# Optimization experiments

Measured on AMD Instinct MI355X. Metric: run time of the kernel, lower is better.

Reference implementation:

```python
import jax, jax.numpy as jnp
import numpy as np

N_VISITS, N_PROC, N_MED = 64, 32, 16
V_DIAG, V_PROC, V_MED = 2000, 1500, 4000
EMB, EMB_FF = 256, 128


def _normalize(adj):
    # row-normalize(adj + I), matching GCN.normalize
    adj = adj + np.eye(adj.shape[0], dtype=np.float32)
    rs = adj.sum(1)
    rinv = np.where(rs > 0, 1.0 / rs, 0.0).astype(np.float32)
    return (adj * rinv[:, None]).astype(np.float32)


def setup_inputs() -> dict:
    key = jax.random.key(0)
    ks = jax.random.split(key, 24)
    rng = np.random.default_rng(0)
    ehr = (rng.random((V_MED, V_MED)) < 0.01).astype(np.float32)
    ddi = (rng.random((V_MED, V_MED)) < 0.01).astype(np.float32)
    s = 0.02
    return {
        'proc_codes': jax.random.randint(ks[0], (N_VISITS, N_PROC), 0, V_DIAG + V_PROC + 2),
        'med_codes': jax.random.randint(ks[1], (N_VISITS, N_MED), 0, V_MED),
        'emb_table': jax.random.normal(ks[2], (V_DIAG + V_PROC + 2, EMB_FF)) * s,
        'conv_w': jax.random.normal(ks[3], (3,)) * 0.3,
        'conv_b': jnp.zeros((1,)),
        'wq': jax.random.normal(ks[4], (EMB_FF, EMB)) * s,
        'wk': jax.random.normal(ks[5], (EMB_FF, EMB)) * s,
        'wv': jax.random.normal(ks[6], (EMB_FF, EMB)) * s,
        'wr': jax.random.normal(ks[7], (EMB, EMB)) * s,
        'alpha': jax.random.normal(ks[8], (EMB,)),
        'beta': jax.random.normal(ks[9], (EMB,)),
        'ehr_adj_norm': jnp.asarray(_normalize(ehr)),
        'ddi_adj_norm': jnp.asarray(_normalize(ddi)),
        'ddi_adj_raw': jnp.asarray(ddi),
        'ehr_w1': jax.random.normal(ks[10], (V_MED, EMB)) * s,
        'ehr_b1': jnp.zeros((EMB,)),
        'ehr_w2': jax.random.normal(ks[11], (EMB, EMB)) * s,
        'ehr_b2': jnp.zeros((EMB,)),
        'ddi_w1': jax.random.normal(ks[12], (V_MED, EMB)) * s,
        'ddi_b1': jnp.zeros((EMB,)),
        'ddi_w2': jax.random.normal(ks[13], (EMB, EMB)) * s,
        'ddi_b2': jnp.zeros((EMB,)),
        'inter': jax.random.normal(ks[14], (1,)) * 0.1,
        'out_w1': jax.random.normal(ks[15], (3 * EMB, 2 * EMB)) * s,
        'out_b1': jnp.zeros((2 * EMB,)),
        'out_w2': jax.random.normal(ks[16], (2 * EMB, V_MED)) * s,
        'out_b2': jnp.zeros((V_MED,)),
    }


def _fastformer(x, wq, wk, wv, wr, alpha, beta):
    # x: (1, n, EMB_FF); additive linear attention (all-ones mask => no-op)
    q = x @ wq  # (1, n, EMB)
    k = x @ wk
    v = x @ wv
    scale = EMB ** -0.5
    aw = jax.nn.softmax(q * alpha * scale, axis=-1)
    gq = jnp.sum(q * aw, axis=1)              # global query (1, EMB)
    p = gq[:, None, :] * k                    # (1, n, EMB)
    bw = jax.nn.softmax(p * beta * scale, axis=-1)
    gk = jnp.sum(p * bw, axis=1)              # global key (1, EMB)
    return (gk[:, None, :] * v) @ wr + q


def _gcn(adj, w1, b1, w2, b2):
    # input x = I, so first layer support is just w1
    h = jax.nn.relu(adj @ w1 + b1)
    return adj @ (h @ w2) + b2


def reference(proc_codes, med_codes, emb_table, conv_w, conv_b, wq, wk, wv, wr, alpha, beta,
              ehr_adj_norm, ddi_adj_norm, ddi_adj_raw,
              ehr_w1, ehr_b1, ehr_w2, ehr_b2, ddi_w1, ddi_b1, ddi_w2, ddi_b2,
              inter, out_w1, out_b1, out_w2, out_b2):
    n = proc_codes.shape[0]
    # per-admission mean embedding  (n, EMB_FF)
    i2 = emb_table[proc_codes].mean(axis=1)
    # Conv1d(1,1,k=3,same) over the feature dim, then ReLU
    xp = jnp.pad(i2, ((0, 0), (1, 1)))
    i2 = jax.nn.relu(conv_w[0] * xp[:, :-2] + conv_w[1] * xp[:, 1:-1] + conv_w[2] * xp[:, 2:] + conv_b)
    feat = _fastformer(i2[None], wq, wk, wv, wr, alpha, beta)[0]  # (n, EMB)
    query = feat[-1:]
    drug_memory = _gcn(ehr_adj_norm, ehr_w1, ehr_b1, ehr_w2, ehr_b2) \
        - _gcn(ddi_adj_norm, ddi_w1, ddi_b1, ddi_w2, ddi_b2) * inter[0]
    key_w1 = jax.nn.softmax(query @ drug_memory.T, axis=-1)   # (1, V_MED)
    fact1 = key_w1 @ drug_memory                              # (1, EMB)
    # history (len(input) > 1): multi-hot med history values
    history_keys = feat[:-1]
    hv = jnp.zeros((n - 1, V_MED), dtype=feat.dtype)
    hv = hv.at[jnp.arange(n - 1)[:, None], med_codes[:-1]].set(1.0)
    visit_w = jax.nn.softmax(query @ history_keys.T, axis=-1)
    fact2 = (visit_w @ hv) @ drug_memory
    h = jnp.concatenate([query, fact1, fact2], axis=-1)       # (1, 3*EMB)
    result = jax.nn.relu(h @ out_w1 + out_b1) @ out_w2 + out_b2
    sp = jax.nn.sigmoid(result)[0]
    batch_neg = 0.0005 * jnp.einsum('i,ij,j->', sp, ddi_adj_raw, sp)
    return result, batch_neg
```

## Files before the change

### kernel.cpp

```cpp
#include <hip/hip_runtime.h>
#include <hip/hip_bf16.h>

#define NV 64
#define NP 32
#define NM 16
#define VMED 4000
#define EMB 256
#define EMBFF 128
#define CAP 128


__device__ __forceinline__ float block_sum_256(float v, float* red) {
    int t = threadIdx.x;
    red[t] = v; __syncthreads();
    for (int s = 128; s > 0; s >>= 1) { if (t < s) red[t] += red[t + s]; __syncthreads(); }
    float r = red[0]; __syncthreads();
    return r;
}
__device__ __forceinline__ float block_max_256(float v, float* red) {
    int t = threadIdx.x;
    red[t] = v; __syncthreads();
    for (int s = 128; s > 0; s >>= 1) { if (t < s) red[t] = fmaxf(red[t], red[t + s]); __syncthreads(); }
    float r = red[0]; __syncthreads();
    return r;
}

__global__ void k_ff1(const int* __restrict__ proc, const float* __restrict__ emb,
                      const float* __restrict__ cw, const float* __restrict__ cb,
                      const float* __restrict__ wq, const float* __restrict__ wk,
                      const float* __restrict__ wv, const float* __restrict__ alpha,
                      float* __restrict__ q, float* __restrict__ k, float* __restrict__ v,
                      float* __restrict__ qaw) {
    __shared__ float sm[EMBFF + 2];
    __shared__ float x[EMBFF];
    __shared__ float red[256];
    int vi = blockIdx.x, t = threadIdx.x;
    if (t < EMBFF) {
        float s = 0.f;
        for (int c = 0; c < NP; c++) s += emb[proc[vi * NP + c] * EMBFF + t];
        sm[t + 1] = s * (1.0f / NP);
    }
    if (t == 0) { sm[0] = 0.f; sm[EMBFF + 1] = 0.f; }
    __syncthreads();
    if (t < EMBFF) {
        float o = cw[0] * sm[t] + cw[1] * sm[t + 1] + cw[2] * sm[t + 2] + cb[0];
        x[t] = o > 0.f ? o : 0.f;
    }
    __syncthreads();
    float aq = 0, ak = 0, av = 0;
    for (int e = 0; e < EMBFF; e++) {
        float xe = x[e];
        aq += xe * wq[e * EMB + t];
        ak += xe * wk[e * EMB + t];
        av += xe * wv[e * EMB + t];
    }
    q[vi * EMB + t] = aq; k[vi * EMB + t] = ak; v[vi * EMB + t] = av;
    const float scale = 0.0625f;
    float z = aq * alpha[t] * scale;
    float m = block_max_256(z, red);
    float e_ = __expf(z - m);
    float sum = block_sum_256(e_, red);
    qaw[vi * EMB + t] = aq * (e_ / sum);
}

__global__ void k_pbw(const float* __restrict__ qaw, const float* __restrict__ k,
                      const float* __restrict__ beta, float* __restrict__ pbw) {
    __shared__ float red[256];
    int vi = blockIdx.x, f = threadIdx.x;
    float g = 0;
    for (int r = 0; r < NV; r++) g += qaw[r * EMB + f];
    float p = g * k[vi * EMB + f];
    const float scale = 0.0625f;
    float z = p * beta[f] * scale;
    float m = block_max_256(z, red);
    float e_ = __expf(z - m);
    float sum = block_sum_256(e_, red);
    pbw[vi * EMB + f] = p * (e_ / sum);
}

__global__ void k_feat(const float* __restrict__ pbw, const float* __restrict__ v,
                       const float* __restrict__ q, const float* __restrict__ wr,
                       float* __restrict__ feat) {
    __shared__ float s[EMB];
    int vi = blockIdx.x, f = threadIdx.x;
    float g = 0;
    for (int r = 0; r < NV; r++) g += pbw[r * EMB + f];
    s[f] = g * v[vi * EMB + f];
    __syncthreads();
    float acc = 0;
    for (int e = 0; e < EMB; e++) acc += s[e] * wr[e * EMB + f];
    feat[vi * EMB + f] = acc + q[vi * EMB + f];
}

__global__ void k_visitw_wmed(const float* __restrict__ feat, const int* __restrict__ med,
                              float* __restrict__ w_med) {
    __shared__ float qs[EMB];
    __shared__ float vw[64];
    __shared__ float red[256];
    __shared__ float wm[VMED];
    int t = threadIdx.x;
    for (int e = t; e < EMB; e += 256) qs[e] = feat[63 * EMB + e];
    for (int i = t; i < VMED; i += 256) wm[i] = 0.f;
    __syncthreads();
    float sc = -1e30f;
    if (t < 63) {
        float a = 0;
        for (int e = 0; e < EMB; e++) a += qs[e] * feat[t * EMB + e];
        sc = a;
    }
    float m = block_max_256(sc, red);
    float e_ = (t < 63) ? __expf(sc - m) : 0.f;
    float sum = block_sum_256(e_, red);
    if (t < 63) vw[t] = e_ / sum;
    __syncthreads();
    for (int i = t; i < 63 * NM; i += 256) {
        int vv = i / NM, mm = i % NM;
        int code = med[vv * NM + mm];
        bool dup = false;
        for (int m2 = 0; m2 < mm; m2++)
            if (med[vv * NM + m2] == code) dup = true;
        if (!dup) atomicAdd(&wm[code], vw[vv]);
    }
    __syncthreads();
    for (int i = t; i < VMED; i += 256) w_med[i] = wm[i];
}

__global__ void k_gcn(const float* __restrict__ eadj, const float* __restrict__ dadj,
                      const float* __restrict__ ew1, const float* __restrict__ eb1,
                      const float* __restrict__ ew2,
                      const float* __restrict__ dw1, const float* __restrict__ db1,
                      const float* __restrict__ dw2,
                      float* __restrict__ outE, float* __restrict__ outD,
                      int* __restrict__ ccntE, int* __restrict__ cidxE, float* __restrict__ cvalE,
                      int* __restrict__ ccntD, int* __restrict__ cidxD, float* __restrict__ cvalD) {
    __shared__ float x[8][EMB];
    __shared__ int idx[CAP];
    __shared__ float val[CAP];
    __shared__ int cnt;
    int b = blockIdx.x, t = threadIdx.x;
    bool isD = b >= 500;
    const float* adj = isD ? dadj : eadj;
    const float* w1  = isD ? dw1  : ew1;
    const float* b1  = isD ? db1  : eb1;
    const float* w2  = isD ? dw2  : ew2;
    float* outp = isD ? outD : outE;
    int*   ccnt = isD ? ccntD : ccntE;
    int*   cidx = isD ? cidxD : cidxE;
    float* cval = isD ? cvalD : cvalE;
    int r0 = (isD ? b - 500 : b) * 8;
    for (int r = 0; r < 8; r++) {
        int i = r0 + r;
        if (t == 0) cnt = 0;
        __syncthreads();
        const float4* row4 = (const float4*)(adj + (size_t)i * VMED);
        for (int j4 = t; j4 < VMED / 4; j4 += 256) {
            float4 a = row4[j4];
            if (a.x != 0.f) { int p = atomicAdd(&cnt, 1); if (p < CAP) { idx[p] = 4*j4+0; val[p] = a.x; } }
            if (a.y != 0.f) { int p = atomicAdd(&cnt, 1); if (p < CAP) { idx[p] = 4*j4+1; val[p] = a.y; } }
            if (a.z != 0.f) { int p = atomicAdd(&cnt, 1); if (p < CAP) { idx[p] = 4*j4+2; val[p] = a.z; } }
            if (a.w != 0.f) { int p = atomicAdd(&cnt, 1); if (p < CAP) { idx[p] = 4*j4+3; val[p] = a.w; } }
        }
        __syncthreads();
        int n = cnt < CAP ? cnt : CAP;
        if (t == 0) ccnt[i] = n;
        if (t < n) { cidx[i * CAP + t] = idx[t]; cval[i * CAP + t] = val[t]; }
        float acc = b1[t];
        for (int e = 0; e < n; e++) acc += val[e] * w1[idx[e] * EMB + t];
        x[r][t] = acc > 0.f ? acc : 0.f;
        __syncthreads();
    }
    float a[8] = {0, 0, 0, 0, 0, 0, 0, 0};
    #pragma unroll 4
    for (int e = 0; e < EMB; e++) {
        float we = w2[e * EMB + t];
        #pragma unroll
        for (int r = 0; r < 8; r++) a[r] += x[r][e] * we;
    }
    for (int r = 0; r < 8; r++) outp[(size_t)(r0 + r) * EMB + t] = a[r];
}

__global__ void k_acc(const int* __restrict__ ccntE, const int* __restrict__ cidxE,
                      const float* __restrict__ cvalE,
                      const int* __restrict__ ccntD, const int* __restrict__ cidxD,
                      const float* __restrict__ cvalD,
                      const float* __restrict__ xe, const float* __restrict__ xd,
                      const float* __restrict__ b2e, const float* __restrict__ b2d,
                      const float* __restrict__ inter, float* __restrict__ dm) {
    __shared__ int idx[CAP];
    __shared__ float val[CAP];
    int i = blockIdx.x, t = threadIdx.x;
    int nE = ccntE[i];
    if (t < nE) { idx[t] = cidxE[i * CAP + t]; val[t] = cvalE[i * CAP + t]; }
    __syncthreads();
    float aE = b2e[t];
    for (int e = 0; e < nE; e++) aE += val[e] * xe[(size_t)idx[e] * EMB + t];
    __syncthreads();
    int nD = ccntD[i];
    if (t < nD) { idx[t] = cidxD[i * CAP + t]; val[t] = cvalD[i * CAP + t]; }
    __syncthreads();
    float aD = b2d[t];
    for (int e = 0; e < nD; e++) aD += val[e] * xd[(size_t)idx[e] * EMB + t];
    dm[(size_t)i * EMB + t] = aE - inter[0] * aD;
}

__global__ void k_scores(const float* __restrict__ dm, const float* __restrict__ feat,
                         float* __restrict__ s_dm) {
    __shared__ float red[256];
    int i = blockIdx.x, t = threadIdx.x;
    float s = dm[(size_t)i * EMB + t] * feat[63 * EMB + t];
    s = block_sum_256(s, red);
    if (t == 0) s_dm[i] = s;
}

__global__ void k_softmax4000(const float* __restrict__ s, float* __restrict__ out) {
    __shared__ float red[256];
    int t = threadIdx.x;
    float m = -1e30f;
    for (int i = t; i < VMED; i += 256) m = fmaxf(m, s[i]);
    m = block_max_256(m, red);
    float sum = 0;
    for (int i = t; i < VMED; i += 256) { float e = __expf(s[i] - m); out[i] = e; sum += e; }
    sum = block_sum_256(sum, red);
    float inv = 1.f / sum;
    for (int i = t; i < VMED; i += 256) out[i] *= inv;
}

__global__ void k_facts_part(const float* __restrict__ dm, const float* __restrict__ kw,
                             const float* __restrict__ wm, float* __restrict__ part1,
                             float* __restrict__ part2) {
    int f = threadIdx.x, b = blockIdx.x;
    int r0 = b * 100;
    float a1 = 0, a2 = 0;
    for (int r = r0; r < r0 + 100; r++) {
        float d = dm[(size_t)r * EMB + f];
        a1 += kw[r] * d;
        a2 += wm[r] * d;
    }
    part1[b * EMB + f] = a1;
    part2[b * EMB + f] = a2;
}

__global__ void k_hidden_part(const float* __restrict__ feat, const float* __restrict__ part1,
                              const float* __restrict__ part2, const float* __restrict__ w1,
                              float* __restrict__ hpart) {
    __shared__ float xs[16];
    int b = blockIdx.x, t = threadIdx.x;
    int e0 = b * 16;
    if (t < 16) {
        int e = e0 + t;
        float xv;
        if (e < 256) xv = feat[63 * EMB + e];
        else if (e < 512) { float s = 0; for (int p = 0; p < 40; p++) s += part1[p * EMB + (e - 256)]; xv = s; }
        else              { float s = 0; for (int p = 0; p < 40; p++) s += part2[p * EMB + (e - 512)]; xv = s; }
        xs[t] = xv;
    }
    __syncthreads();
    float a1 = 0, a2 = 0;
    #pragma unroll
    for (int i = 0; i < 16; i++) {
        int e = e0 + i;
        a1 += xs[i] * w1[e * 512 + t];
        a2 += xs[i] * w1[e * 512 + t + 256];
    }
    hpart[b * 512 + t] = a1;
    hpart[b * 512 + t + 256] = a2;
}

__global__ void k_result(const float* __restrict__ hpart, const float* __restrict__ b1,
                         const float* __restrict__ w2, const float* __restrict__ b2,
                         float* __restrict__ out, float* __restrict__ sp) {
    __shared__ float hx[512];
    __shared__ float red[8][32];
    int t = threadIdx.x;
    for (int jj = t; jj < 512; jj += 256) {
        float s = b1[jj];
        for (int p = 0; p < 48; p++) s += hpart[p * 512 + jj];
        hx[jj] = s > 0.f ? s : 0.f;
    }
    __syncthreads();
    int lane = t & 31, seg = t >> 5;
    int j = blockIdx.x * 32 + lane;
    float acc = 0;
    int e0 = seg * 64;
    #pragma unroll 8
    for (int e = e0; e < e0 + 64; e++) acc += hx[e] * w2[(size_t)e * VMED + j];
    red[seg][lane] = acc;
    __syncthreads();
    if (seg == 0) {
        float s = b2[j];
        for (int p = 0; p < 8; p++) s += red[p][lane];
        out[j] = s;
        sp[j] = 1.f / (1.f + __expf(-s));
    }
}

__global__ void k_bneg(const float* __restrict__ ddi, const float* __restrict__ sp,
                       float* __restrict__ bpart) {
    __shared__ float4 spl[VMED / 4];
    __shared__ float red[256];
    int t = threadIdx.x;
    const float4* sp4 = (const float4*)sp;
    for (int j4 = t; j4 < VMED / 4; j4 += 256) spl[j4] = sp4[j4];
    __syncthreads();
    for (int rr = 0; rr < 8; rr++) {
        int i = blockIdx.x * 8 + rr;
        const float4* row4 = (const float4*)(ddi + (size_t)i * VMED);
        float p = 0;
        for (int j4 = t; j4 < VMED / 4; j4 += 256) {
            float4 a = row4[j4];
            float4 s4 = spl[j4];
            p += a.x * s4.x + a.y * s4.y + a.z * s4.z + a.w * s4.w;
        }
        p = block_sum_256(p, red);
        if (t == 0) bpart[i] = sp[i] * p;
    }
}

__global__ void FastRx_wo_Diag_19473381720179_kernel(const float* __restrict__ bpart,
                                                     float* __restrict__ out) {
    __shared__ float red[256];
    int t = threadIdx.x;
    float s = 0;
    for (int i = t; i < VMED; i += 256) s += bpart[i];
    s = block_sum_256(s, red);
    if (t == 0) out[VMED] = 0.0005f * s;
}

extern "C" __attribute__((visibility("default")))
void kernel_launch(void* const* d_in, const int* in_sizes, int n_in,
                   void* d_out, int out_size, void* d_ws, size_t ws_size,
                   hipStream_t stream) {
    const int*   proc_codes = (const int*)d_in[0];
    const int*   med_codes  = (const int*)d_in[1];
    const float* emb_table  = (const float*)d_in[2];
    const float* conv_w     = (const float*)d_in[3];
    const float* conv_b     = (const float*)d_in[4];
    const float* wq         = (const float*)d_in[5];
    const float* wk         = (const float*)d_in[6];
    const float* wv         = (const float*)d_in[7];
    const float* wr         = (const float*)d_in[8];
    const float* alpha      = (const float*)d_in[9];
    const float* beta       = (const float*)d_in[10];
    const float* ehr_adj    = (const float*)d_in[11];
    const float* ddi_adj    = (const float*)d_in[12];
    const float* ddi_raw    = (const float*)d_in[13];
    const float* ehr_w1     = (const float*)d_in[14];
    const float* ehr_b1     = (const float*)d_in[15];
    const float* ehr_w2     = (const float*)d_in[16];
    const float* ehr_b2     = (const float*)d_in[17];
    const float* ddi_w1     = (const float*)d_in[18];
    const float* ddi_b1     = (const float*)d_in[19];
    const float* ddi_w2     = (const float*)d_in[20];
    const float* ddi_b2     = (const float*)d_in[21];
    const float* inter      = (const float*)d_in[22];
    const float* out_w1     = (const float*)d_in[23];
    const float* out_b1     = (const float*)d_in[24];
    const float* out_w2     = (const float*)d_in[25];
    const float* out_b2     = (const float*)d_in[26];
    float* out = (float*)d_out;

    float* w = (float*)d_ws;
    float* q      = w;
    float* k      = w + 16384;
    float* v      = w + 32768;
    float* tmpA   = w + 49152;
    float* tmpB   = w + 65536;
    float* feat   = w + 81920;
    float* wmed   = w + 98304;
    float* sdm    = w + 102400;
    float* sp     = w + 106496;
    float* bufA   = w + 110592;
    float* bufC   = bufA + 1024000;
    float* bufB   = bufC + 1024000;
    int*   ccntE  = (int*)(bufB + 1024000);
    int*   cidxE  = ccntE + 4096;
    float* cvalE  = (float*)(cidxE + 512000);
    int*   ccntD  = (int*)(cvalE + 512000);
    int*   cidxD  = ccntD + 4096;
    float* cvalD  = (float*)(cidxD + 512000);
    float* part1  = bufA;
    float* part2  = bufA + 10240;
    float* hpart  = bufA + 20480;
    float* bpart  = bufA + 45056;

    k_ff1<<<NV, EMB, 0, stream>>>(proc_codes, emb_table, conv_w, conv_b,
                                  wq, wk, wv, alpha, q, k, v, tmpA);
    k_pbw<<<NV, EMB, 0, stream>>>(tmpA, k, beta, tmpB);
    k_feat<<<NV, EMB, 0, stream>>>(tmpB, v, q, wr, feat);
    k_visitw_wmed<<<1, 256, 0, stream>>>(feat, med_codes, wmed);

    k_gcn<<<1000, 256, 0, stream>>>(ehr_adj, ddi_adj,
                                    ehr_w1, ehr_b1, ehr_w2,
                                    ddi_w1, ddi_b1, ddi_w2,
                                    bufA, bufC,
                                    ccntE, cidxE, cvalE, ccntD, cidxD, cvalD);
    k_acc<<<VMED, 256, 0, stream>>>(ccntE, cidxE, cvalE, ccntD, cidxD, cvalD,
                                    bufA, bufC, ehr_b2, ddi_b2, inter, bufB);

    k_scores<<<VMED, 256, 0, stream>>>(bufB, feat, sdm);
    k_softmax4000<<<1, 256, 0, stream>>>(sdm, sdm);
    k_facts_part<<<40, 256, 0, stream>>>(bufB, sdm, wmed, part1, part2);
    k_hidden_part<<<48, 256, 0, stream>>>(feat, part1, part2, out_w1, hpart);
    k_result<<<125, 256, 0, stream>>>(hpart, out_b1, out_w2, out_b2, out, sp);
    k_bneg<<<VMED / 8, 256, 0, stream>>>(ddi_raw, sp, bpart);
    FastRx_wo_Diag_19473381720179_kernel<<<1, 256, 0, stream>>>(bpart, out);
}
```

Measured before the change: 431.1 us.

## Scan all eight adjacency rows together in GCN and fuse score reduction into accumulation

The GCN kernel now compacts the nonzeros of all eight adjacency rows in one pass, using per-row shared counters and buffers. This removes the per-row barriers and the serialized row-by-row scans, giving more memory parallelism per block. The score dot product with the query is also folded into the k_acc kernel, which removes the separate k_scores launch and its re-read of drug memory. The cost is more shared memory per block, which may lower occupancy.

```diff
diff --git a/kernel.cpp b/kernel.cpp
--- a/kernel.cpp
+++ b/kernel.cpp
@@ -134,9 +134,9 @@
                       int* __restrict__ ccntE, int* __restrict__ cidxE, float* __restrict__ cvalE,
                       int* __restrict__ ccntD, int* __restrict__ cidxD, float* __restrict__ cvalD) {
     __shared__ float x[8][EMB];
-    __shared__ int idx[CAP];
-    __shared__ float val[CAP];
-    __shared__ int cnt;
+    __shared__ int idx[8][CAP];
+    __shared__ float val[8][CAP];
+    __shared__ int cnt[8];
     int b = blockIdx.x, t = threadIdx.x;
     bool isD = b >= 500;
     const float* adj = isD ? dadj : eadj;
@@ -148,27 +148,29 @@
     int*   cidx = isD ? cidxD : cidxE;
     float* cval = isD ? cvalD : cvalE;
     int r0 = (isD ? b - 500 : b) * 8;
+    if (t < 8) cnt[t] = 0;
+    __syncthreads();
+    const float4* base4 = (const float4*)(adj + (size_t)r0 * VMED);
+    const int Q = VMED / 4;
+    for (int jj = t; jj < 8 * Q; jj += 256) {
+        float4 a = base4[jj];
+        int r = jj / Q;
+        int c0 = (jj - r * Q) * 4;
+        if (a.x != 0.f) { int p = atomicAdd(&cnt[r], 1); if (p < CAP) { idx[r][p] = c0;     val[r][p] = a.x; } }
+        if (a.y != 0.f) { int p = atomicAdd(&cnt[r], 1); if (p < CAP) { idx[r][p] = c0 + 1; val[r][p] = a.y; } }
+        if (a.z != 0.f) { int p = atomicAdd(&cnt[r], 1); if (p < CAP) { idx[r][p] = c0 + 2; val[r][p] = a.z; } }
+        if (a.w != 0.f) { int p = atomicAdd(&cnt[r], 1); if (p < CAP) { idx[r][p] = c0 + 3; val[r][p] = a.w; } }
+    }
+    __syncthreads();
     for (int r = 0; r < 8; r++) {
-        int i = r0 + r;
-        if (t == 0) cnt = 0;
-        __syncthreads();
-        const float4* row4 = (const float4*)(adj + (size_t)i * VMED);
-        for (int j4 = t; j4 < VMED / 4; j4 += 256) {
-            float4 a = row4[j4];
-            if (a.x != 0.f) { int p = atomicAdd(&cnt, 1); if (p < CAP) { idx[p] = 4*j4+0; val[p] = a.x; } }
-            if (a.y != 0.f) { int p = atomicAdd(&cnt, 1); if (p < CAP) { idx[p] = 4*j4+1; val[p] = a.y; } }
-            if (a.z != 0.f) { int p = atomicAdd(&cnt, 1); if (p < CAP) { idx[p] = 4*j4+2; val[p] = a.z; } }
-            if (a.w != 0.f) { int p = atomicAdd(&cnt, 1); if (p < CAP) { idx[p] = 4*j4+3; val[p] = a.w; } }
-        }
-        __syncthreads();
-        int n = cnt < CAP ? cnt : CAP;
-        if (t == 0) ccnt[i] = n;
-        if (t < n) { cidx[i * CAP + t] = idx[t]; cval[i * CAP + t] = val[t]; }
+        int n = cnt[r] < CAP ? cnt[r] : CAP;
+        if (t == 0) ccnt[r0 + r] = n;
+        if (t < n) { cidx[(r0 + r) * CAP + t] = idx[r][t]; cval[(r0 + r) * CAP + t] = val[r][t]; }
         float acc = b1[t];
-        for (int e = 0; e < n; e++) acc += val[e] * w1[idx[e] * EMB + t];
+        for (int e = 0; e < n; e++) acc += val[r][e] * w1[idx[r][e] * EMB + t];
         x[r][t] = acc > 0.f ? acc : 0.f;
-        __syncthreads();
-    }
+    }
+    __syncthreads();
     float a[8] = {0, 0, 0, 0, 0, 0, 0, 0};
     #pragma unroll 4
     for (int e = 0; e < EMB; e++) {
@@ -185,9 +187,11 @@
                       const float* __restrict__ cvalD,
                       const float* __restrict__ xe, const float* __restrict__ xd,
                       const float* __restrict__ b2e, const float* __restrict__ b2d,
-                      const float* __restrict__ inter, float* __restrict__ dm) {
+                      const float* __restrict__ inter, const float* __restrict__ feat,
+                      float* __restrict__ dm, float* __restrict__ sdm) {
     __shared__ int idx[CAP];
     __shared__ float val[CAP];
+    __shared__ float red[256];
     int i = blockIdx.x, t = threadIdx.x;
     int nE = ccntE[i];
     if (t < nE) { idx[t] = cidxE[i * CAP + t]; val[t] = cvalE[i * CAP + t]; }
@@ -200,16 +204,10 @@
     __syncthreads();
     float aD = b2d[t];
     for (int e = 0; e < nD; e++) aD += val[e] * xd[(size_t)idx[e] * EMB + t];
-    dm[(size_t)i * EMB + t] = aE - inter[0] * aD;
-}
-
-__global__ void k_scores(const float* __restrict__ dm, const float* __restrict__ feat,
-                         float* __restrict__ s_dm) {
-    __shared__ float red[256];
-    int i = blockIdx.x, t = threadIdx.x;
-    float s = dm[(size_t)i * EMB + t] * feat[63 * EMB + t];
-    s = block_sum_256(s, red);
-    if (t == 0) s_dm[i] = s;
+    float dmv = aE - inter[0] * aD;
+    dm[(size_t)i * EMB + t] = dmv;
+    float s = block_sum_256(dmv * feat[63 * EMB + t], red);
+    if (t == 0) sdm[i] = s;
 }
 
 __global__ void k_softmax4000(const float* __restrict__ s, float* __restrict__ out) {
@@ -395,9 +393,9 @@
                                     bufA, bufC,
                                     ccntE, cidxE, cvalE, ccntD, cidxD, cvalD);
     k_acc<<<VMED, 256, 0, stream>>>(ccntE, cidxE, cvalE, ccntD, cidxD, cvalD,
-                                    bufA, bufC, ehr_b2, ddi_b2, inter, bufB);
-
-    k_scores<<<VMED, 256, 0, stream>>>(bufB, feat, sdm);
+                                    bufA, bufC, ehr_b2, ddi_b2, inter, feat,
+                                    bufB, sdm);
+
     k_softmax4000<<<1, 256, 0, stream>>>(sdm, sdm);
     k_facts_part<<<40, 256, 0, stream>>>(bufB, sdm, wmed, part1, part2);
     k_hidden_part<<<48, 256, 0, stream>>>(feat, part1, part2, out_w1, hpart);
```

Result: no change. 426.9 us (-1.0%).
